# Performance work log

Hardware: AMD Instinct MI355X
Metric: run time of the kernel (lower is better)

The kernel has to match this reference:

```python
import jax, jax.numpy as jnp
import numpy as np
import math

B, M, C, H = 4, 2048, 512, 8
DQK = C // 4 // H  # 16 per-head query/key dim


def setup_inputs() -> dict:
    key = jax.random.key(0)
    ks = jax.random.split(key, 8)
    s = 0.02
    return {
        "x": jax.random.normal(ks[0], (B, M, C), dtype=jnp.float32),
        "mask": jax.random.randint(ks[1], (B, M), 0, 2, dtype=jnp.int32),
        "Wq": jax.random.normal(ks[2], (C, C // 4), dtype=jnp.float32) * s,
        "bq": jnp.zeros((C // 4,), dtype=jnp.float32),
        "Wk": jax.random.normal(ks[3], (C, C // 4), dtype=jnp.float32) * s,
        "bk": jnp.zeros((C // 4,), dtype=jnp.float32),
        "Wv": jax.random.normal(ks[4], (C, C), dtype=jnp.float32) * s,
        "bv": jnp.zeros((C,), dtype=jnp.float32),
        "gamma": jnp.ones((1,), dtype=jnp.float32),
    }


def reference(x, mask, Wq, bq, Wk, bk, Wv, bv, gamma):
    b, m, c = x.shape
    # projections, split heads: q/k -> (B, H, M, DQK), v -> (B, H, M, C//H)
    q = (x @ Wq + bq).reshape(b, m, H, -1).transpose(0, 2, 1, 3)
    k = (x @ Wk + bk).reshape(b, m, H, -1).transpose(0, 2, 1, 3)
    v = (x @ Wv + bv).reshape(b, m, H, -1).transpose(0, 2, 1, 3)
    scale = 1.0 / math.sqrt(q.shape[-1])
    scores = jnp.einsum('bhmd,bhnd->bhmn', q, k) * scale
    beta = jax.nn.softmax(jax.nn.relu(scores), axis=-1)  # act='relu' pre-softmax
    # att_drop = 0.0 -> identity
    mf = mask.astype(x.dtype)[:, None, None, :]  # (B,1,1,M)
    beta = beta * mf
    beta = beta / (beta.sum(-1, keepdims=True) + 1e-12)
    o = gamma * jnp.einsum('bhmn,bhnd->bhmd', beta, v)  # (B,H,M,C//H)
    return o.transpose(0, 2, 1, 3).reshape(b, m, c)
```

## Files before the change

### kernel.cpp

```cpp
#include <hip/hip_runtime.h>
#include <hip/hip_bf16.h>

#define MSEQ 2048

typedef __attribute__((ext_vector_type(8))) short short8;
typedef __attribute__((ext_vector_type(4))) short short4v;
typedef __attribute__((ext_vector_type(4))) float f32x4;

static __device__ __forceinline__ short bf16b(float f) {
    __hip_bfloat16 h = __float2bfloat16(f);
    return *reinterpret_cast<short*>(&h);
}

static __device__ __forceinline__ float fast_exp2(float x) {
    float r;
    asm("v_exp_f32 %0, %1" : "=v"(r) : "v"(x));
    return r;
}

static __device__ __forceinline__ f32x4 mfma16(short4v a, short4v b, f32x4 c) {
    return __builtin_amdgcn_mfma_f32_16x16x16bf16_1k(a, b, c, 0, 0, 0);
}

static __device__ __forceinline__ void gl_lds16(const void* g, void* l) {
    __builtin_amdgcn_global_load_lds(
        (const __attribute__((address_space(1))) unsigned int*)g,
        (__attribute__((address_space(3))) unsigned int*)l, 16, 0, 0);
}

__global__ __launch_bounds__(256) void xcvt_kernel(
    const float* __restrict__ x, unsigned short* __restrict__ xb)
{
    const size_t i = ((size_t)blockIdx.x * 256 + threadIdx.x) * 8;
    const float4 a = *(const float4*)(x + i);
    const float4 b = *(const float4*)(x + i + 4);
    short8 o;
    o[0]=bf16b(a.x); o[1]=bf16b(a.y); o[2]=bf16b(a.z); o[3]=bf16b(a.w);
    o[4]=bf16b(b.x); o[5]=bf16b(b.y); o[6]=bf16b(b.z); o[7]=bf16b(b.w);
    *(short8*)(xb + i) = o;
}

__global__ __launch_bounds__(256) void wtrans_kernel(
    const float* __restrict__ Wq, const float* __restrict__ Wk,
    const float* __restrict__ Wv, unsigned short* __restrict__ WT)
{
    const int nt = blockIdx.x;
    const int kt = blockIdx.y;
    const int t  = threadIdx.x;
    const int k0 = kt*64;

    const float* W; int ld, n0;
    if (nt < 2)      { W = Wq; ld = 128; n0 = nt*64; }
    else if (nt < 4) { W = Wk; ld = 128; n0 = (nt-2)*64; }
    else             { W = Wv; ld = 512; n0 = (nt-4)*64; }

    __shared__ unsigned short Ts[64*72];

    #pragma unroll
    for (int s = 0; s < 4; ++s) {
        const int lin = s*256 + t;
        const int krow = lin >> 4, ng = lin & 15;
        const float4 v = *(const float4*)(W + (size_t)(k0+krow)*ld + n0 + ng*4);
        Ts[(ng*4+0)*72 + krow] = (unsigned short)bf16b(v.x);
        Ts[(ng*4+1)*72 + krow] = (unsigned short)bf16b(v.y);
        Ts[(ng*4+2)*72 + krow] = (unsigned short)bf16b(v.z);
        Ts[(ng*4+3)*72 + krow] = (unsigned short)bf16b(v.w);
    }
    __syncthreads();
    #pragma unroll
    for (int s = 0; s < 2; ++s) {
        const int lin = s*256 + t;
        const int nrow = lin >> 3, kg = lin & 7;
        *(short8*)(WT + (size_t)(nt*64 + nrow)*512 + k0 + kg*8) = *(const short8*)&Ts[nrow*72 + kg*8];
    }
}

__global__ __launch_bounds__(256, 3) void proj_mfma(
    const unsigned short* __restrict__ xb, const unsigned short* __restrict__ WT,
    const float* __restrict__ bq, const float* __restrict__ bk, const float* __restrict__ bv,
    unsigned short* __restrict__ Qb, unsigned short* __restrict__ Kb, unsigned short* __restrict__ Vt)
{
    const int nt = blockIdx.x;
    const int r0 = blockIdx.y * 64;
    const int n0 = nt * 128;
    const int t = threadIdx.x, w = t >> 6, lane = t & 63, l15 = lane & 15, quad = lane >> 4;
    const int qh = w >> 1, chh = w & 1;

    __shared__ short smem[128*72];
    short* As = smem;
    short* Bs = smem + 64*32;

    f32x4 acc[2][4];
    #pragma unroll
    for (int i = 0; i < 2; ++i)
        #pragma unroll
        for (int j = 0; j < 4; ++j) acc[i][j] = {0.f,0.f,0.f,0.f};

    const int arow = lane >> 2, akg = lane & 3;

    for (int kk = 0; kk < 512; kk += 32) {
        gl_lds16(xb + (size_t)(r0 + w*16 + arow)*512 + kk + akg*8, As + (w*16)*32);
        gl_lds16(WT + (size_t)(n0 + w*16 + arow)*512 + kk + akg*8, Bs + (w*16)*32);
        gl_lds16(WT + (size_t)(n0 + 64 + w*16 + arow)*512 + kk + akg*8, Bs + (64 + w*16)*32);
        __syncthreads();
        short8 Af[2], Bf[4];
        #pragma unroll
        for (int i = 0; i < 2; ++i) Af[i] = *(const short8*)&As[(qh*32 + i*16 + l15)*32 + quad*8];
        #pragma unroll
        for (int j = 0; j < 4; ++j) Bf[j] = *(const short8*)&Bs[(chh*64 + j*16 + l15)*32 + quad*8];
        #pragma unroll
        for (int i = 0; i < 2; ++i)
            #pragma unroll
            for (int j = 0; j < 4; ++j)
                acc[i][j] = __builtin_amdgcn_mfma_f32_16x16x32_bf16(Af[i], Bf[j], acc[i][j], 0, 0, 0);
        __syncthreads();
    }

    const float* bias = (nt == 0) ? bq : (nt == 1) ? bk : (bv + (nt-2)*128);
    const float kscale = (nt == 1) ? 0.36067376022224085f : 1.0f;
    float bj[4];
    #pragma unroll
    for (int j = 0; j < 4; ++j) bj[j] = bias[chh*64 + j*16 + l15];

    short* Ts = smem;
    if (nt < 2) {
        #pragma unroll
        for (int i = 0; i < 2; ++i)
            #pragma unroll
            for (int j = 0; j < 4; ++j)
                #pragma unroll
                for (int r = 0; r < 4; ++r)
                    Ts[(qh*32 + i*16 + quad*4 + r)*136 + chh*64 + j*16 + l15] =
                        bf16b((acc[i][j][r] + bj[j]) * kscale);
    } else {
        #pragma unroll
        for (int i = 0; i < 2; ++i)
            #pragma unroll
            for (int j = 0; j < 4; ++j)
                #pragma unroll
                for (int r = 0; r < 4; ++r)
                    Ts[(chh*64 + j*16 + l15)*72 + qh*32 + i*16 + quad*4 + r] =
                        bf16b(acc[i][j][r] + bj[j]);
    }
    __syncthreads();

    if (nt < 2) {
        unsigned short* Out = (nt == 0) ? Qb : Kb;
        #pragma unroll
        for (int s = 0; s < 4; ++s) {
            const int lin = s*256 + t, row = lin >> 4, seg = lin & 15;
            *(short8*)(Out + (size_t)(r0+row)*128 + seg*8) = *(const short8*)&Ts[row*136 + seg*8];
        }
    } else {
        const int b = r0 >> 11, key0 = r0 & 2047, chBase = (nt-2)*128;
        #pragma unroll
        for (int s = 0; s < 4; ++s) {
            const int lin = s*256 + t, row = lin >> 3, seg = lin & 7;
            *(short8*)(Vt + ((size_t)(b*512 + chBase + row))*MSEQ + key0 + seg*8) =
                *(const short8*)&Ts[row*72 + seg*8];
        }
    }
}

__global__ __launch_bounds__(256, 4) void attn_mfma(
    const unsigned short* __restrict__ Qb, const unsigned short* __restrict__ Kb,
    const unsigned short* __restrict__ Vt, const int* __restrict__ mask,
    const float* __restrict__ gamma, float* __restrict__ out)
{
    const int bid = blockIdx.y * 32 + blockIdx.x;
    const int lin = (bid & 7) * 128 + (bid >> 3);
    const int mt = lin & 31;
    const int bh = lin >> 5;
    const int b  = bh >> 3, h = bh & 7;
    const int m0 = mt * 64;
    const int t  = threadIdx.x;
    const int w = t >> 6, lane = t & 63, l15 = lane & 15, quad = lane >> 4;
    const int mq = m0 + w*16;

    __shared__ __align__(16) short Ks[2][64*16];
    __shared__ __align__(16) short Vs[2][64*64];
    __shared__ __align__(16) int   Ms[2][64];

    const short4v qf = *(const short4v*)(Qb + (size_t)(b*MSEQ + mq + l15)*128 + h*16 + quad*4);

    const unsigned short* Kg = Kb + (size_t)(b*MSEQ + (lane>>1))*128 + h*16
                                  + (((lane&1) ^ ((lane>>3)&1))*8);
    const int vj0 = 2*w;
    const unsigned short* Vg0 = Vt + (size_t)(b*512 + h*64 + vj0*8 + (lane>>3))*MSEQ
                                   + (((lane&7) ^ ((lane>>3)&7)) * 8);
    const unsigned short* Vg1 = Vg0 + (size_t)8*MSEQ;
    const int* Mg = mask + b*MSEQ + lane*4;

#define ATT_STAGE(bufi, kn)                                                   \
  {                                                                           \
    gl_lds16(Vg0 + (kn), &Vs[bufi][vj0*512]);                                 \
    gl_lds16(Vg1 + (kn), &Vs[bufi][(vj0+1)*512]);                             \
    if (w == 0) {                                                             \
      gl_lds16(Kg + (size_t)(kn)*128,      &Ks[bufi][0]);                     \
      gl_lds16(Kg + (size_t)((kn)+32)*128, &Ks[bufi][32*16]);                 \
    }                                                                         \
    if (w == 1 && lane < 16) gl_lds16(Mg + (kn), &Ms[bufi][0]);               \
  }

    f32x4 O[4];
    #pragma unroll
    for (int v = 0; v < 4; ++v) O[v] = {0.f,0.f,0.f,0.f};
    float ws = 0.f;

    ATT_STAGE(0, 0)
    asm volatile("s_waitcnt vmcnt(0)" ::: "memory");
    __syncthreads();

    for (int kt = 0; kt < 32; ++kt) {
        const int cur = kt & 1;
        if (kt < 31) ATT_STAGE(cur ^ 1, (kt+1)*64)

        const short* Kc = Ks[cur];
        const short* Vc = Vs[cur];
        const int*   Mc = Ms[cur];

        #pragma unroll
        for (int s = 0; s < 4; ++s) {
            const int krow = s*16 + l15;
            const int kg = ((quad>>1) ^ ((krow>>2)&1));
            const short4v kf = *(const short4v*)&Kc[krow*16 + kg*8 + (quad&1)*4];
            const int4 mk = *(const int4*)&Mc[s*16 + quad*4];
            f32x4 sc = {0.f,0.f,0.f,0.f};
            sc = mfma16(kf, qf, sc);
            const float w0 = mk.x ? fast_exp2(fmaxf(sc[0], 0.f)) : 0.f;
            const float w1 = mk.y ? fast_exp2(fmaxf(sc[1], 0.f)) : 0.f;
            const float w2 = mk.z ? fast_exp2(fmaxf(sc[2], 0.f)) : 0.f;
            const float w3 = mk.w ? fast_exp2(fmaxf(sc[3], 0.f)) : 0.f;
            ws += (w0 + w1) + (w2 + w3);
            short4v pf;
            pf[0]=bf16b(w0); pf[1]=bf16b(w1); pf[2]=bf16b(w2); pf[3]=bf16b(w3);
            #pragma unroll
            for (int v = 0; v < 4; ++v) {
                const int ch = v*16 + l15;
                const int g = (2*s + (quad>>1)) ^ (ch & 7);
                const short4v vf = *(const short4v*)&Vc[ch*64 + g*8 + (quad&1)*4];
                O[v] = mfma16(pf, vf, O[v]);
            }
        }
        asm volatile("s_waitcnt vmcnt(0)" ::: "memory");
        __syncthreads();
    }

    ws += __shfl_xor(ws, 16, 64);
    ws += __shfl_xor(ws, 32, 64);
    const float g = gamma[0];
    float inv[4];
    #pragma unroll
    for (int r = 0; r < 4; ++r)
        inv[r] = g / fmaxf(__shfl(ws, quad*4 + r, 64), 1e-20f);

    float* op = out + (size_t)(b*MSEQ + mq + quad*4)*512 + h*64 + l15;
    #pragma unroll
    for (int r = 0; r < 4; ++r) {
        op[(size_t)r*512 +  0] = O[0][r] * inv[r];
        op[(size_t)r*512 + 16] = O[1][r] * inv[r];
        op[(size_t)r*512 + 32] = O[2][r] * inv[r];
        op[(size_t)r*512 + 48] = O[3][r] * inv[r];
    }
#undef ATT_STAGE
}

extern "C" void kernel_launch(void* const* d_in, const int* in_sizes, int n_in,
                              void* d_out, int out_size, void* d_ws, size_t ws_size,
                              hipStream_t stream) {
    const float* x     = (const float*)d_in[0];
    const int*   mask  = (const int*)  d_in[1];
    const float* Wq    = (const float*)d_in[2];
    const float* bq    = (const float*)d_in[3];
    const float* Wk    = (const float*)d_in[4];
    const float* bk    = (const float*)d_in[5];
    const float* Wv    = (const float*)d_in[6];
    const float* bv    = (const float*)d_in[7];
    const float* gamma = (const float*)d_in[8];
    float* outp = (float*)d_out;

    unsigned short* xb = (unsigned short*)d_ws;
    unsigned short* WT = xb + (size_t)8192*512;
    unsigned short* Qb = WT + (size_t)768*512;
    unsigned short* Kb = Qb + (size_t)8192*128;
    unsigned short* Vt = Kb + (size_t)8192*128;

    xcvt_kernel<<<2048, 256, 0, stream>>>(x, xb);
    wtrans_kernel<<<dim3(12, 8), 256, 0, stream>>>(Wq, Wk, Wv, WT);
    proj_mfma<<<dim3(6, 128), 256, 0, stream>>>(xb, WT, bq, bk, bv, Qb, Kb, Vt);
    attn_mfma<<<dim3(32, 32), 256, 0, stream>>>(Qb, Kb, Vt, mask, gamma, outp);
}
```

Baseline: 156.4 us.

## Fold mask into V and compute masked row sums via MFMA, double-buffer projection

Multiplies V rows by the key mask inside the projection epilogue, so the attention loop no longer selects on the mask per element. Masked row sums are computed by an extra MFMA against a bf16 mask vector that a merged prep kernel builds. The change also merges the x-convert and weight-transpose kernels into one launch, double-buffers the projection K-loop, and precomputes LDS offsets. The risks are bf16 rounding of the row sums, since P is rounded before the sum, and the removal of the explicit vmcnt waits before the barriers.

```diff
diff --git a/kernel.cpp b/kernel.cpp
--- a/kernel.cpp
+++ b/kernel.cpp
@@ -28,33 +28,46 @@
         (__attribute__((address_space(3))) unsigned int*)l, 16, 0, 0);
 }
 
-__global__ __launch_bounds__(256) void xcvt_kernel(
-    const float* __restrict__ x, unsigned short* __restrict__ xb)
+__global__ __launch_bounds__(256) void prep_kernel(
+    const float* __restrict__ x, unsigned short* __restrict__ xb,
+    const float* __restrict__ Wq, const float* __restrict__ Wk,
+    const float* __restrict__ Wv, unsigned short* __restrict__ WT,
+    const int* __restrict__ mask, unsigned short* __restrict__ maskbf)
 {
-    const size_t i = ((size_t)blockIdx.x * 256 + threadIdx.x) * 8;
-    const float4 a = *(const float4*)(x + i);
-    const float4 b = *(const float4*)(x + i + 4);
-    short8 o;
-    o[0]=bf16b(a.x); o[1]=bf16b(a.y); o[2]=bf16b(a.z); o[3]=bf16b(a.w);
-    o[4]=bf16b(b.x); o[5]=bf16b(b.y); o[6]=bf16b(b.z); o[7]=bf16b(b.w);
-    *(short8*)(xb + i) = o;
-}
-
-__global__ __launch_bounds__(256) void wtrans_kernel(
-    const float* __restrict__ Wq, const float* __restrict__ Wk,
-    const float* __restrict__ Wv, unsigned short* __restrict__ WT)
-{
-    const int nt = blockIdx.x;
-    const int kt = blockIdx.y;
-    const int t  = threadIdx.x;
+    __shared__ unsigned short Ts[64*72];
+    const int bid = blockIdx.x;
+    const int t = threadIdx.x;
+
+    if (bid < 2048) {
+        const size_t i = ((size_t)bid * 256 + t) * 8;
+        const float4 a = *(const float4*)(x + i);
+        const float4 b = *(const float4*)(x + i + 4);
+        short8 o;
+        o[0]=bf16b(a.x); o[1]=bf16b(a.y); o[2]=bf16b(a.z); o[3]=bf16b(a.w);
+        o[4]=bf16b(b.x); o[5]=bf16b(b.y); o[6]=bf16b(b.z); o[7]=bf16b(b.w);
+        *(short8*)(xb + i) = o;
+        return;
+    }
+    if (bid == 2144) {
+        #pragma unroll
+        for (int j = 0; j < 8; ++j) {
+            const int4 m4 = *(const int4*)(mask + (t*8 + j)*4);
+            short4v o;
+            o[0]=bf16b((float)m4.x); o[1]=bf16b((float)m4.y);
+            o[2]=bf16b((float)m4.z); o[3]=bf16b((float)m4.w);
+            *(short4v*)(maskbf + (t*8 + j)*4) = o;
+        }
+        return;
+    }
+    const int idx = bid - 2048;
+    const int nt = idx >> 3;
+    const int kt = idx & 7;
     const int k0 = kt*64;
 
     const float* W; int ld, n0;
     if (nt < 2)      { W = Wq; ld = 128; n0 = nt*64; }
     else if (nt < 4) { W = Wk; ld = 128; n0 = (nt-2)*64; }
     else             { W = Wv; ld = 512; n0 = (nt-4)*64; }
-
-    __shared__ unsigned short Ts[64*72];
 
     #pragma unroll
     for (int s = 0; s < 4; ++s) {
@@ -78,6 +91,7 @@
 __global__ __launch_bounds__(256, 3) void proj_mfma(
     const unsigned short* __restrict__ xb, const unsigned short* __restrict__ WT,
     const float* __restrict__ bq, const float* __restrict__ bk, const float* __restrict__ bv,
+    const int* __restrict__ mask,
     unsigned short* __restrict__ Qb, unsigned short* __restrict__ Kb, unsigned short* __restrict__ Vt)
 {
     const int nt = blockIdx.x;
@@ -86,9 +100,9 @@
     const int t = threadIdx.x, w = t >> 6, lane = t & 63, l15 = lane & 15, quad = lane >> 4;
     const int qh = w >> 1, chh = w & 1;
 
-    __shared__ short smem[128*72];
+    __shared__ short smem[12288];
     short* As = smem;
-    short* Bs = smem + 64*32;
+    short* Bs = smem + 4096;
 
     f32x4 acc[2][4];
     #pragma unroll
@@ -98,16 +112,29 @@
 
     const int arow = lane >> 2, akg = lane & 3;
 
-    for (int kk = 0; kk < 512; kk += 32) {
-        gl_lds16(xb + (size_t)(r0 + w*16 + arow)*512 + kk + akg*8, As + (w*16)*32);
-        gl_lds16(WT + (size_t)(n0 + w*16 + arow)*512 + kk + akg*8, Bs + (w*16)*32);
-        gl_lds16(WT + (size_t)(n0 + 64 + w*16 + arow)*512 + kk + akg*8, Bs + (64 + w*16)*32);
-        __syncthreads();
+#define PROJ_STAGE(BUFI, KK) {                                                          \
+    gl_lds16(xb + (size_t)(r0 + w*16 + arow)*512 + (KK) + akg*8,                        \
+             (char*)As + (BUFI)*4096 + w*1024);                                         \
+    gl_lds16(WT + (size_t)(n0 + w*16 + arow)*512 + (KK) + akg*8,                        \
+             (char*)Bs + (BUFI)*8192 + w*1024);                                         \
+    gl_lds16(WT + (size_t)(n0 + 64 + w*16 + arow)*512 + (KK) + akg*8,                   \
+             (char*)Bs + (BUFI)*8192 + 4096 + w*1024);                                  \
+}
+
+    PROJ_STAGE(0, 0)
+    __syncthreads();
+
+    #pragma unroll 1
+    for (int kp = 0; kp < 16; ++kp) {
+        const int cur = kp & 1;
+        if (kp < 15) PROJ_STAGE(cur ^ 1, (kp+1)*32)
         short8 Af[2], Bf[4];
         #pragma unroll
-        for (int i = 0; i < 2; ++i) Af[i] = *(const short8*)&As[(qh*32 + i*16 + l15)*32 + quad*8];
-        #pragma unroll
-        for (int j = 0; j < 4; ++j) Bf[j] = *(const short8*)&Bs[(chh*64 + j*16 + l15)*32 + quad*8];
+        for (int i = 0; i < 2; ++i)
+            Af[i] = *(const short8*)&As[cur*2048 + (qh*32 + i*16 + l15)*32 + quad*8];
+        #pragma unroll
+        for (int j = 0; j < 4; ++j)
+            Bf[j] = *(const short8*)&Bs[cur*4096 + (chh*64 + j*16 + l15)*32 + quad*8];
         #pragma unroll
         for (int i = 0; i < 2; ++i)
             #pragma unroll
@@ -122,6 +149,7 @@
     #pragma unroll
     for (int j = 0; j < 4; ++j) bj[j] = bias[chh*64 + j*16 + l15];
 
+    const int bb = r0 >> 11, key0 = r0 & 2047;
     short* Ts = smem;
     if (nt < 2) {
         #pragma unroll
@@ -133,6 +161,12 @@
                     Ts[(qh*32 + i*16 + quad*4 + r)*136 + chh*64 + j*16 + l15] =
                         bf16b((acc[i][j][r] + bj[j]) * kscale);
     } else {
+        float mv[2][4];
+        #pragma unroll
+        for (int i = 0; i < 2; ++i)
+            #pragma unroll
+            for (int r = 0; r < 4; ++r)
+                mv[i][r] = (float)mask[bb*MSEQ + key0 + qh*32 + i*16 + quad*4 + r];
         #pragma unroll
         for (int i = 0; i < 2; ++i)
             #pragma unroll
@@ -140,7 +174,7 @@
                 #pragma unroll
                 for (int r = 0; r < 4; ++r)
                     Ts[(chh*64 + j*16 + l15)*72 + qh*32 + i*16 + quad*4 + r] =
-                        bf16b(acc[i][j][r] + bj[j]);
+                        bf16b((acc[i][j][r] + bj[j]) * mv[i][r]);
     }
     __syncthreads();
 
@@ -152,25 +186,25 @@
             *(short8*)(Out + (size_t)(r0+row)*128 + seg*8) = *(const short8*)&Ts[row*136 + seg*8];
         }
     } else {
-        const int b = r0 >> 11, key0 = r0 & 2047, chBase = (nt-2)*128;
+        const int chBase = (nt-2)*128;
         #pragma unroll
         for (int s = 0; s < 4; ++s) {
             const int lin = s*256 + t, row = lin >> 3, seg = lin & 7;
-            *(short8*)(Vt + ((size_t)(b*512 + chBase + row))*MSEQ + key0 + seg*8) =
+            *(short8*)(Vt + ((size_t)(bb*512 + chBase + row))*MSEQ + key0 + seg*8) =
                 *(const short8*)&Ts[row*72 + seg*8];
         }
     }
+#undef PROJ_STAGE
 }
 
 __global__ __launch_bounds__(256, 4) void attn_mfma(
     const unsigned short* __restrict__ Qb, const unsigned short* __restrict__ Kb,
-    const unsigned short* __restrict__ Vt, const int* __restrict__ mask,
+    const unsigned short* __restrict__ Vt, const unsigned short* __restrict__ maskbf,
     const float* __restrict__ gamma, float* __restrict__ out)
 {
     const int bid = blockIdx.y * 32 + blockIdx.x;
     const int lin = (bid & 7) * 128 + (bid >> 3);
-    const int mt = lin & 31;
-    const int bh = lin >> 5;
+    const int mt = lin & 31, bh = lin >> 5;
     const int b  = bh >> 3, h = bh & 7;
     const int m0 = mt * 64;
     const int t  = threadIdx.x;
@@ -179,80 +213,80 @@
 
     __shared__ __align__(16) short Ks[2][64*16];
     __shared__ __align__(16) short Vs[2][64*64];
-    __shared__ __align__(16) int   Ms[2][64];
+    __shared__ __align__(16) short Msb[2][64];
 
     const short4v qf = *(const short4v*)(Qb + (size_t)(b*MSEQ + mq + l15)*128 + h*16 + quad*4);
 
     const unsigned short* Kg = Kb + (size_t)(b*MSEQ + (lane>>1))*128 + h*16
-                                  + (((lane&1) ^ ((lane>>3)&1))*8);
+                              + (((lane&1) ^ ((lane>>3)&1))*8);
     const int vj0 = 2*w;
     const unsigned short* Vg0 = Vt + (size_t)(b*512 + h*64 + vj0*8 + (lane>>3))*MSEQ
-                                   + (((lane&7) ^ ((lane>>3)&7)) * 8);
+                               + (((lane&7) ^ ((lane>>3)&7)) * 8);
     const unsigned short* Vg1 = Vg0 + (size_t)8*MSEQ;
-    const int* Mg = mask + b*MSEQ + lane*4;
-
-#define ATT_STAGE(bufi, kn)                                                   \
-  {                                                                           \
-    gl_lds16(Vg0 + (kn), &Vs[bufi][vj0*512]);                                 \
-    gl_lds16(Vg1 + (kn), &Vs[bufi][(vj0+1)*512]);                             \
-    if (w == 0) {                                                             \
-      gl_lds16(Kg + (size_t)(kn)*128,      &Ks[bufi][0]);                     \
-      gl_lds16(Kg + (size_t)((kn)+32)*128, &Ks[bufi][32*16]);                 \
-    }                                                                         \
-    if (w == 1 && lane < 16) gl_lds16(Mg + (kn), &Ms[bufi][0]);               \
-  }
+    const unsigned short* Mgb = maskbf + b*MSEQ + lane*8;
+
+#define ATT_STAGE(BUFI, KN) {                                                       \
+    gl_lds16(Vg0 + (KN), &Vs[BUFI][vj0*512]);                                       \
+    gl_lds16(Vg1 + (KN), &Vs[BUFI][(vj0+1)*512]);                                   \
+    if (w < 2)          gl_lds16(Kg + (size_t)((KN) + w*32)*128, &Ks[BUFI][w*32*16]);\
+    else if (lane < 8)  gl_lds16(Mgb + (KN), &Msb[BUFI][0]);                        \
+}
+
+    const char* KsB = (const char*)&Ks[0][0];
+    const char* VsB = (const char*)&Vs[0][0];
+    const char* MsB = (const char*)&Msb[0][0];
+    const int kofs = l15*32 + (((quad>>1) ^ ((l15>>2)&1))*16) + (quad&1)*8;
+    const int mofs = quad*8;
+    int vb[4];
+    #pragma unroll
+    for (int v = 0; v < 4; ++v) {
+        const int ch = v*16 + l15;
+        vb[v] = ch*128 + (((quad>>1) ^ (ch&7))*16) + (quad&1)*8;
+    }
 
     f32x4 O[4];
     #pragma unroll
     for (int v = 0; v < 4; ++v) O[v] = {0.f,0.f,0.f,0.f};
-    float ws = 0.f;
+    f32x4 WS = {0.f,0.f,0.f,0.f};
 
     ATT_STAGE(0, 0)
-    asm volatile("s_waitcnt vmcnt(0)" ::: "memory");
     __syncthreads();
 
+    #pragma unroll 1
     for (int kt = 0; kt < 32; ++kt) {
         const int cur = kt & 1;
         if (kt < 31) ATT_STAGE(cur ^ 1, (kt+1)*64)
 
-        const short* Kc = Ks[cur];
-        const short* Vc = Vs[cur];
-        const int*   Mc = Ms[cur];
+        const char* Kc = KsB + cur*2048;
+        const char* Vc = VsB + cur*8192;
+        const char* Mc = MsB + cur*128;
 
         #pragma unroll
         for (int s = 0; s < 4; ++s) {
-            const int krow = s*16 + l15;
-            const int kg = ((quad>>1) ^ ((krow>>2)&1));
-            const short4v kf = *(const short4v*)&Kc[krow*16 + kg*8 + (quad&1)*4];
-            const int4 mk = *(const int4*)&Mc[s*16 + quad*4];
+            const short4v kf  = *(const short4v*)(Kc + kofs + s*512);
+            const short4v mkf = *(const short4v*)(Mc + mofs + s*32);
             f32x4 sc = {0.f,0.f,0.f,0.f};
             sc = mfma16(kf, qf, sc);
-            const float w0 = mk.x ? fast_exp2(fmaxf(sc[0], 0.f)) : 0.f;
-            const float w1 = mk.y ? fast_exp2(fmaxf(sc[1], 0.f)) : 0.f;
-            const float w2 = mk.z ? fast_exp2(fmaxf(sc[2], 0.f)) : 0.f;
-            const float w3 = mk.w ? fast_exp2(fmaxf(sc[3], 0.f)) : 0.f;
-            ws += (w0 + w1) + (w2 + w3);
+            const float w0 = fast_exp2(fmaxf(sc[0], 0.f));
+            const float w1 = fast_exp2(fmaxf(sc[1], 0.f));
+            const float w2 = fast_exp2(fmaxf(sc[2], 0.f));
+            const float w3 = fast_exp2(fmaxf(sc[3], 0.f));
             short4v pf;
             pf[0]=bf16b(w0); pf[1]=bf16b(w1); pf[2]=bf16b(w2); pf[3]=bf16b(w3);
+            WS = mfma16(pf, mkf, WS);
             #pragma unroll
             for (int v = 0; v < 4; ++v) {
-                const int ch = v*16 + l15;
-                const int g = (2*s + (quad>>1)) ^ (ch & 7);
-                const short4v vf = *(const short4v*)&Vc[ch*64 + g*8 + (quad&1)*4];
+                const short4v vf = *(const short4v*)(Vc + (vb[v] ^ (s*32)));
                 O[v] = mfma16(pf, vf, O[v]);
             }
         }
-        asm volatile("s_waitcnt vmcnt(0)" ::: "memory");
         __syncthreads();
     }
 
-    ws += __shfl_xor(ws, 16, 64);
-    ws += __shfl_xor(ws, 32, 64);
     const float g = gamma[0];
     float inv[4];
     #pragma unroll
-    for (int r = 0; r < 4; ++r)
-        inv[r] = g / fmaxf(__shfl(ws, quad*4 + r, 64), 1e-20f);
+    for (int r = 0; r < 4; ++r) inv[r] = g / fmaxf(WS[r], 1e-20f);
 
     float* op = out + (size_t)(b*MSEQ + mq + quad*4)*512 + h*64 + l15;
     #pragma unroll
@@ -284,9 +318,9 @@
     unsigned short* Qb = WT + (size_t)768*512;
     unsigned short* Kb = Qb + (size_t)8192*128;
     unsigned short* Vt = Kb + (size_t)8192*128;
-
-    xcvt_kernel<<<2048, 256, 0, stream>>>(x, xb);
-    wtrans_kernel<<<dim3(12, 8), 256, 0, stream>>>(Wq, Wk, Wv, WT);
-    proj_mfma<<<dim3(6, 128), 256, 0, stream>>>(xb, WT, bq, bk, bv, Qb, Kb, Vt);
-    attn_mfma<<<dim3(32, 32), 256, 0, stream>>>(Qb, Kb, Vt, mask, gamma, outp);
-}
+    unsigned short* maskbf = Vt + (size_t)2048*MSEQ;
+
+    prep_kernel<<<2145, 256, 0, stream>>>(x, xb, Wq, Wk, Wv, WT, mask, maskbf);
+    proj_mfma<<<dim3(6, 128), 256, 0, stream>>>(xb, WT, bq, bk, bv, mask, Qb, Kb, Vt);
+    attn_mfma<<<dim3(32, 32), 256, 0, stream>>>(Qb, Kb, Vt, maskbf, gamma, outp);
+}
```

Result: faster. 152.8 us (-2.3%).
